# Kernel optimization log

Measured on AMD Instinct MI355X. Metric: run time of the kernel, lower is better.

Reference implementation:

```python
import jax, jax.numpy as jnp
import numpy as np

IN_FEATURES = 4096
OUT_FEATURES = 4096
NUM_GROUPS = 32
HARDTANH_MIN = -2.0
HARDTANH_MAX = 2.0
EPS = 1e-6


def setup_inputs() -> dict:
    key = jax.random.key(0)
    k1, k2 = jax.random.split(key)
    x = jax.random.normal(k1, (8192, IN_FEATURES), dtype=jnp.float32)
    W = jax.random.normal(k2, (OUT_FEATURES, IN_FEATURES), dtype=jnp.float32)
    b = jnp.zeros((OUT_FEATURES,), dtype=jnp.float32)
    return {"x": x, "W": W, "b": b}


def reference(x, W, b):
    B = x.shape[0]
    group_size = OUT_FEATURES // NUM_GROUPS
    # GEMM: y[b, n] = sum_k x[b, k] * W[n, k]
    y = jnp.einsum("bk,nk->bn", x, W)
    # GroupNorm over each group of channels per row (no affine scale)
    yg = y.reshape(B, NUM_GROUPS, group_size)
    mean = jnp.mean(yg, axis=2, keepdims=True)
    var = jnp.mean((yg - mean) ** 2, axis=2, keepdims=True)
    norm = (yg - mean) / jnp.sqrt(var + EPS)
    norm = norm.reshape(B, OUT_FEATURES) + b[None, :]
    # kernel clamps to [-2, 2], then outer clamp to [hardtanh_min, hardtanh_max]
    out = jnp.clip(norm, -2.0, 2.0)
    out = jnp.clip(out, HARDTANH_MIN, HARDTANH_MAX)
    return out
```

## Files before the change

### kernel.cpp

```cpp
#include <hip/hip_runtime.h>
#include <hip/hip_bf16.h>
#include <stdint.h>

#define M_DIM 8192
#define N_DIM 4096
#define K_DIM 4096
#define BM 256
#define BN 256
#define BK 64
#define NTL 64

typedef __attribute__((ext_vector_type(8))) short short8;
typedef __attribute__((ext_vector_type(4))) float f32x4;
typedef unsigned short ushort_t;

#define SBAR()   __builtin_amdgcn_s_barrier()
#define LGKM(n)  asm volatile("s_waitcnt lgkmcnt(" #n ")")
#define VMF(n)   asm volatile("s_waitcnt vmcnt(" #n ")" ::: "memory")

__device__ __forceinline__ ushort_t f2bf(float f) {
    uint32_t u = __float_as_uint(f);
    uint32_t r = (u + 0x7FFFu + ((u >> 16) & 1u)) >> 16;
    return (ushort_t)r;
}

__global__ void cvt_f32_bf16(const float4* __restrict__ in, ushort* __restrict__ out4, int n4) {
    int i = blockIdx.x * blockDim.x + threadIdx.x;
    if (i < n4) {
        float4 v = in[i];
        ushort_t a = f2bf(v.x), b = f2bf(v.y), c = f2bf(v.z), d = f2bf(v.w);
        uint32_t lo = (uint32_t)a | ((uint32_t)b << 16);
        uint32_t hi = (uint32_t)c | ((uint32_t)d << 16);
        uint2* o = reinterpret_cast<uint2*>(out4);
        o[i] = make_uint2(lo, hi);
    }
}

__device__ __forceinline__ void gload_lds16(const ushort_t* g, void* l) {
    __builtin_amdgcn_global_load_lds(
        (const __attribute__((address_space(1))) unsigned int*)g,
        (__attribute__((address_space(3))) unsigned int*)l,
        16, 0, 0);
}

__global__ __launch_bounds__(512, 2)
void gemm_gn_kernel(const ushort_t* __restrict__ xb,
                    const ushort_t* __restrict__ wb,
                    const float*   __restrict__ bias,
                    float*         __restrict__ out)
{
    __shared__ char pool[131072];

    const int tid = threadIdx.x;
    const int w   = tid >> 6;
    const int l   = tid & 63;
    const int wr  = w >> 2;
    const int wc  = w & 3;
    const int l15 = l & 15;
    const int l4  = l >> 4;

    const int TN = N_DIM / BN;
    int bid = blockIdx.x;
    bid = (bid & 7) * 64 + (bid >> 3);
    const int brow = (bid / TN) * BM;
    const int bcol = (bid % TN) * BN;

    const int srow8 = tid >> 3;
    const int sslot = (tid & 7) ^ (srow8 & 7);
    const ushort_t* gA = xb + (size_t)(brow + srow8) * K_DIM + sslot * 8;
    const ushort_t* gB = wb + (size_t)(bcol + srow8) * K_DIM + sslot * 8;
    const size_t ROW64 = (size_t)64 * K_DIM;
    const int w1024 = w * 1024;

    auto STAGE_A = [&](int buf, int half, int kt) {
        const ushort_t* s = gA + (size_t)half * 128 * K_DIM + (size_t)kt * 64;
        char* d = pool + buf * 65536 + half * 16384 + w1024;
        gload_lds16(s,         d);
        gload_lds16(s + ROW64, d + 8192);
    };
    auto STAGE_B = [&](int buf, int half, int kt) {
        const ushort_t* s = gB + (size_t)half * 128 * K_DIM + (size_t)kt * 64;
        char* d = pool + buf * 65536 + 32768 + half * 16384 + w1024;
        gload_lds16(s,         d);
        gload_lds16(s + ROW64, d + 8192);
    };

    const int swz = (l15 & 7) << 4;
    const int x0  = (l4 * 16) ^ swz;
    const int x1  = (64 + l4 * 16) ^ swz;

    short8 afL[8], afH[8], bfL[4], bfH[4];

    auto RD_A = [&](short8* dst, const char* Ab, int mi0) {
#pragma unroll
        for (int m = 0; m < 4; ++m) {
            const char* p = Ab + ((mi0 + m) * 32 + wr * 16 + l15) * 128;
            dst[m * 2]     = *(const short8*)(p + x0);
            dst[m * 2 + 1] = *(const short8*)(p + x1);
        }
    };
    auto RD_B = [&](short8* dst, const char* Bb, int ni0) {
#pragma unroll
        for (int n = 0; n < 2; ++n) {
            const char* p = Bb + ((ni0 + n) * 64 + wc * 16 + l15) * 128;
            dst[n * 2]     = *(const short8*)(p + x0);
            dst[n * 2 + 1] = *(const short8*)(p + x1);
        }
    };

    f32x4 acc[8][4];
#pragma unroll
    for (int i = 0; i < 8; ++i)
#pragma unroll
        for (int j = 0; j < 4; ++j) acc[i][j] = (f32x4){0.f, 0.f, 0.f, 0.f};

    auto MM = [&](short8* A, short8* B, int m0, int n0) {
        __builtin_amdgcn_s_setprio(1);
#pragma unroll
        for (int k = 0; k < 2; ++k)
#pragma unroll
            for (int m = 0; m < 4; ++m)
#pragma unroll
                for (int n = 0; n < 2; ++n)
                    acc[m0 + m][n0 + n] = __builtin_amdgcn_mfma_f32_16x16x32_bf16(
                        A[m * 2 + k], B[n * 2 + k], acc[m0 + m][n0 + n], 0, 0, 0);
        __builtin_amdgcn_s_setprio(0);
    };

    STAGE_A(0, 0, 0); STAGE_A(0, 1, 0);
    STAGE_B(0, 0, 0); STAGE_B(0, 1, 0);
    STAGE_A(1, 0, 1); STAGE_A(1, 1, 1);
    STAGE_B(1, 0, 1);
    VMF(6);
    SBAR();

#pragma unroll 2
    for (int T = 0; T < NTL; ++T) {
        const int c = T & 1;
        const char* Ab = pool + c * 65536;
        const char* Bb = Ab + 32768;

        RD_A(afL, Ab, 0);
        RD_B(bfL, Bb, 0);
        if (T + 1 < NTL) STAGE_B(c ^ 1, 1, T + 1);
        LGKM(8);
        SBAR(); LGKM(0);
        MM(afL, bfL, 0, 0);
        SBAR();

        RD_A(afH, Ab, 4);
        if (T + 2 < NTL) STAGE_A(c, 0, T + 2);
        SBAR(); LGKM(0);
        MM(afH, bfL, 4, 0);
        SBAR();

        RD_B(bfH, Bb, 2);
        if (T + 2 < NTL) STAGE_A(c, 1, T + 2);
        SBAR(); LGKM(0);
        MM(afH, bfH, 4, 2);
        SBAR();

        if (T + 2 < NTL) STAGE_B(c, 0, T + 2);
        if (T < NTL - 2) { VMF(6); } else { VMF(0); }
        SBAR();
        MM(afL, bfH, 0, 2);
        SBAR();
    }

    __syncthreads();

    float* redS  = (float*)pool;
    float* redS2 = (float*)(pool + 8192);
#pragma unroll
    for (int mi = 0; mi < 8; ++mi)
#pragma unroll
        for (int r = 0; r < 4; ++r) {
            float gl  = acc[mi][0][r] + acc[mi][1][r];
            float gh  = acc[mi][2][r] + acc[mi][3][r];
            float gl2 = acc[mi][0][r] * acc[mi][0][r] + acc[mi][1][r] * acc[mi][1][r];
            float gh2 = acc[mi][2][r] * acc[mi][2][r] + acc[mi][3][r] * acc[mi][3][r];
#pragma unroll
            for (int m = 1; m < 16; m <<= 1) {
                gl  += __shfl_xor(gl,  m);
                gh  += __shfl_xor(gh,  m);
                gl2 += __shfl_xor(gl2, m);
                gh2 += __shfl_xor(gh2, m);
            }
            if (l15 == 0) {
                int R = mi * 32 + wr * 16 + l4 * 4 + r;
                redS [R * 8 + wc * 2]     = gl;
                redS [R * 8 + wc * 2 + 1] = gh;
                redS2[R * 8 + wc * 2]     = gl2;
                redS2[R * 8 + wc * 2 + 1] = gh2;
            }
        }
    __syncthreads();

    float bv[4];
#pragma unroll
    for (int ni = 0; ni < 4; ++ni)
        bv[ni] = bias[bcol + ni * 64 + wc * 16 + l15];

    const float inv_gs = 1.0f / 128.0f;
#pragma unroll
    for (int mi = 0; mi < 8; ++mi)
#pragma unroll
        for (int r = 0; r < 4; ++r) {
            int R = mi * 32 + wr * 16 + l4 * 4 + r;
            float S0 = redS [R * 8 + 0] + redS [R * 8 + 2] + redS [R * 8 + 4] + redS [R * 8 + 6];
            float S1 = redS [R * 8 + 1] + redS [R * 8 + 3] + redS [R * 8 + 5] + redS [R * 8 + 7];
            float T0 = redS2[R * 8 + 0] + redS2[R * 8 + 2] + redS2[R * 8 + 4] + redS2[R * 8 + 6];
            float T1 = redS2[R * 8 + 1] + redS2[R * 8 + 3] + redS2[R * 8 + 5] + redS2[R * 8 + 7];
            float mean0 = S0 * inv_gs, mean1 = S1 * inv_gs;
            float inv0 = rsqrtf(T0 * inv_gs - mean0 * mean0 + 1e-6f);
            float inv1 = rsqrtf(T1 * inv_gs - mean1 * mean1 + 1e-6f);
            size_t rowbase = (size_t)(brow + R) * N_DIM + bcol + wc * 16 + l15;
#pragma unroll
            for (int ni = 0; ni < 4; ++ni) {
                float mean = (ni < 2) ? mean0 : mean1;
                float inv  = (ni < 2) ? inv0  : inv1;
                float v = (acc[mi][ni][r] - mean) * inv + bv[ni];
                v = fminf(fmaxf(v, -2.0f), 2.0f);
                out[rowbase + ni * 64] = v;
            }
        }
}

extern "C" void kernel_launch(void* const* d_in, const int* in_sizes, int n_in,
                              void* d_out, int out_size, void* d_ws, size_t ws_size,
                              hipStream_t stream) {
    const float* x = (const float*)d_in[0];
    const float* W = (const float*)d_in[1];
    const float* b = (const float*)d_in[2];
    float* out = (float*)d_out;

    ushort_t* xb = (ushort_t*)d_ws;
    ushort_t* wb = xb + (size_t)M_DIM * K_DIM;

    int n4x = M_DIM * K_DIM / 4;
    cvt_f32_bf16<<<(n4x + 255) / 256, 256, 0, stream>>>(
        (const float4*)x, xb, n4x);
    int n4w = N_DIM * K_DIM / 4;
    cvt_f32_bf16<<<(n4w + 255) / 256, 256, 0, stream>>>(
        (const float4*)W, wb, n4w);

    int grid = (M_DIM / BM) * (N_DIM / BN);
    gemm_gn_kernel<<<grid, 512, 0, stream>>>(xb, wb, b, out);
}
```

Before: 323.1 us.

## Restructure GEMM main loop into register double-buffered half-K steps

Replaces the four-quadrant-per-tile loop, which issued several barriers per tile, with 128 half-tile steps. Each step prefetches the next step's full A/B fragments from LDS into a second register set while running 32 MFMAs on the current set. Global-to-LDS staging of a whole tile is issued every other step, and sched_barrier fences keep the compiler from reordering across the phases. The goal is fewer barriers and better overlap of LDS reads with MFMA, at the cost of more fragment registers and a single vmcnt(0) wait every other step.

```diff
diff --git a/kernel.cpp b/kernel.cpp
--- a/kernel.cpp
+++ b/kernel.cpp
@@ -7,16 +7,17 @@
 #define K_DIM 4096
 #define BM 256
 #define BN 256
-#define BK 64
-#define NTL 64
+#define NSTEP 128
+#define NT64 64
 
 typedef __attribute__((ext_vector_type(8))) short short8;
 typedef __attribute__((ext_vector_type(4))) float f32x4;
 typedef unsigned short ushort_t;
 
-#define SBAR()   __builtin_amdgcn_s_barrier()
-#define LGKM(n)  asm volatile("s_waitcnt lgkmcnt(" #n ")")
-#define VMF(n)   asm volatile("s_waitcnt vmcnt(" #n ")" ::: "memory")
+#define SBAR()    __builtin_amdgcn_s_barrier()
+#define SCHEDB()  __builtin_amdgcn_sched_barrier(0)
+#define LGKM0M()  asm volatile("s_waitcnt lgkmcnt(0)" ::: "memory")
+#define VMF(n)    asm volatile("s_waitcnt vmcnt(" #n ")" ::: "memory")
 
 __device__ __forceinline__ ushort_t f2bf(float f) {
     uint32_t u = __float_as_uint(f);
@@ -86,85 +87,63 @@
     };
 
     const int swz = (l15 & 7) << 4;
-    const int x0  = (l4 * 16) ^ swz;
-    const int x1  = (64 + l4 * 16) ^ swz;
-
-    short8 afL[8], afH[8], bfL[4], bfH[4];
-
-    auto RD_A = [&](short8* dst, const char* Ab, int mi0) {
-#pragma unroll
-        for (int m = 0; m < 4; ++m) {
-            const char* p = Ab + ((mi0 + m) * 32 + wr * 16 + l15) * 128;
-            dst[m * 2]     = *(const short8*)(p + x0);
-            dst[m * 2 + 1] = *(const short8*)(p + x1);
+    const int abase = (wr * 16 + l15) * 128;
+    const int bbase = (wc * 16 + l15) * 128;
+
+    auto RDALL = [&](short8* af, short8* bf, int u1) {
+        const char* base = pool + (((u1 >> 1) & 1) << 16);
+        const int xp = ((u1 & 1) * 64 + l4 * 16) ^ swz;
+#pragma unroll
+        for (int mi = 0; mi < 8; ++mi)
+            af[mi] = *(const short8*)(base + abase + mi * 32 * 128 + xp);
+        const char* bb = base + 32768;
+#pragma unroll
+        for (int ni = 0; ni < 4; ++ni)
+            bf[ni] = *(const short8*)(bb + bbase + ni * 64 * 128 + xp);
+    };
+
+    f32x4 acc[8][4];
+#pragma unroll
+    for (int i = 0; i < 8; ++i)
+#pragma unroll
+        for (int j = 0; j < 4; ++j) acc[i][j] = (f32x4){0.f, 0.f, 0.f, 0.f};
+
+    auto STEP = [&](int u, bool vm0, short8* afc, short8* bfc, short8* afn, short8* bfn) {
+        LGKM0M();
+        if (vm0) { VMF(0); }
+        SCHEDB();
+        SBAR();
+        const int ts = (u + 3) >> 1;
+        if ((u & 1) && ts < NT64) {
+            STAGE_A(ts & 1, 0, ts); STAGE_A(ts & 1, 1, ts);
+            STAGE_B(ts & 1, 0, ts); STAGE_B(ts & 1, 1, ts);
         }
-    };
-    auto RD_B = [&](short8* dst, const char* Bb, int ni0) {
-#pragma unroll
-        for (int n = 0; n < 2; ++n) {
-            const char* p = Bb + ((ni0 + n) * 64 + wc * 16 + l15) * 128;
-            dst[n * 2]     = *(const short8*)(p + x0);
-            dst[n * 2 + 1] = *(const short8*)(p + x1);
-        }
-    };
-
-    f32x4 acc[8][4];
-#pragma unroll
-    for (int i = 0; i < 8; ++i)
-#pragma unroll
-        for (int j = 0; j < 4; ++j) acc[i][j] = (f32x4){0.f, 0.f, 0.f, 0.f};
-
-    auto MM = [&](short8* A, short8* B, int m0, int n0) {
+        if (u < NSTEP - 1) RDALL(afn, bfn, u + 1);
         __builtin_amdgcn_s_setprio(1);
 #pragma unroll
-        for (int k = 0; k < 2; ++k)
-#pragma unroll
-            for (int m = 0; m < 4; ++m)
-#pragma unroll
-                for (int n = 0; n < 2; ++n)
-                    acc[m0 + m][n0 + n] = __builtin_amdgcn_mfma_f32_16x16x32_bf16(
-                        A[m * 2 + k], B[n * 2 + k], acc[m0 + m][n0 + n], 0, 0, 0);
+        for (int mi = 0; mi < 8; ++mi)
+#pragma unroll
+            for (int ni = 0; ni < 4; ++ni)
+                acc[mi][ni] = __builtin_amdgcn_mfma_f32_16x16x32_bf16(
+                    afc[mi], bfc[ni], acc[mi][ni], 0, 0, 0);
         __builtin_amdgcn_s_setprio(0);
+        SCHEDB();
     };
 
     STAGE_A(0, 0, 0); STAGE_A(0, 1, 0);
     STAGE_B(0, 0, 0); STAGE_B(0, 1, 0);
     STAGE_A(1, 0, 1); STAGE_A(1, 1, 1);
-    STAGE_B(1, 0, 1);
-    VMF(6);
+    STAGE_B(1, 0, 1); STAGE_B(1, 1, 1);
+    VMF(8);
     SBAR();
 
-#pragma unroll 2
-    for (int T = 0; T < NTL; ++T) {
-        const int c = T & 1;
-        const char* Ab = pool + c * 65536;
-        const char* Bb = Ab + 32768;
-
-        RD_A(afL, Ab, 0);
-        RD_B(bfL, Bb, 0);
-        if (T + 1 < NTL) STAGE_B(c ^ 1, 1, T + 1);
-        LGKM(8);
-        SBAR(); LGKM(0);
-        MM(afL, bfL, 0, 0);
-        SBAR();
-
-        RD_A(afH, Ab, 4);
-        if (T + 2 < NTL) STAGE_A(c, 0, T + 2);
-        SBAR(); LGKM(0);
-        MM(afH, bfL, 4, 0);
-        SBAR();
-
-        RD_B(bfH, Bb, 2);
-        if (T + 2 < NTL) STAGE_A(c, 1, T + 2);
-        SBAR(); LGKM(0);
-        MM(afH, bfH, 4, 2);
-        SBAR();
-
-        if (T + 2 < NTL) STAGE_B(c, 0, T + 2);
-        if (T < NTL - 2) { VMF(6); } else { VMF(0); }
-        SBAR();
-        MM(afL, bfH, 0, 2);
-        SBAR();
+    short8 afA[8], bfA[4], afB[8], bfB[4];
+    RDALL(afA, bfA, 0);
+    SCHEDB();
+
+    for (int s = 0; s < NSTEP / 2; ++s) {
+        STEP(2 * s,     true,  afA, bfA, afB, bfB);
+        STEP(2 * s + 1, false, afB, bfB, afA, bfA);
     }
 
     __syncthreads();
```

After: 320.3 us. No clear change (-0.9%).
